# Kernel optimization log

Hardware: AMD Instinct MI355X
Metric: run time of the kernel (lower is better)

Reference implementation:

```python
import jax, jax.numpy as jnp
import numpy as np

D_MODEL = 1024
D_SAE = 16384
BATCH = 4096
EPS = 1e-8

def _layer_norm(v):
    # v: [B, D]; matches torch branch with keepdim=True
    mean = v.mean(axis=1, keepdims=True)
    var = ((v - mean) ** 2).mean(axis=1, keepdims=True)
    return (v - mean) / jnp.sqrt(var + EPS)

def setup_inputs() -> dict:
    key = jax.random.key(0)
    k1, k2 = jax.random.split(key)
    x = jax.random.normal(k1, (BATCH, 2 * D_MODEL), dtype=jnp.float32)
    # kaiming_uniform on [d_model, d_sae]: bound = sqrt(6 / fan_in), fan_in = d_sae (torch default mode='fan_in' on dim 1)
    bound = float(np.sqrt(6.0 / D_SAE))
    W_enc = jax.random.uniform(k2, (D_MODEL, D_SAE), dtype=jnp.float32, minval=-bound, maxval=bound)
    W_dec = W_enc.T  # init ties decoder to encoder transpose
    b_enc = jnp.zeros((D_SAE,), dtype=jnp.float32)
    b_dec = jnp.zeros((D_MODEL,), dtype=jnp.float32)
    return {"x": x, "W_enc": W_enc, "b_enc": b_enc, "W_dec": W_dec, "b_dec": b_dec, "k": 64}

def reference(x, W_enc, b_enc, W_dec, b_dec, k):
    B = x.shape[0]
    d_model = W_enc.shape[0]
    src = x[:, :d_model]
    tgt = x[:, d_model:]
    # standardize_method == 'layer_norm_and_diff_layer_norm'
    diff = _layer_norm(_layer_norm(tgt) - _layer_norm(src))  # [B, D]
    # encode
    acts = jax.nn.relu(diff @ W_enc + b_enc)  # [B, F]
    # batch top-k on decoder-norm-scaled scores
    dec_norms = jnp.linalg.norm(W_dec, axis=1)  # [F]
    flat_scores = (acts * dec_norms).reshape(-1)  # [B*F]
    _, topk_idx = jax.lax.top_k(flat_scores, k * B)
    mask = jnp.zeros_like(flat_scores).at[topk_idx].set(1.0).reshape(B, -1)
    sparse_acts = acts * mask  # [B, F]
    # decode
    recon = sparse_acts @ W_dec + b_dec  # [B, D]
    return recon
```

## Files before the change

### kernel.cpp

```cpp
#include <hip/hip_runtime.h>
#include <math.h>

#define D_MODEL 1024
#define D_SAE   16384
#define BATCH   4096
#define NTOT    (1ull * BATCH * D_SAE)
#define LN_EPS  1e-8
#define EPS_M   3e-4f
#define ROW_CAP 256
#define CAND_CAP  (4 * 1024 * 1024)
#define CAND2_CAP 65536

using bf16x8 = __attribute__((ext_vector_type(8))) short;
using f32x4  = __attribute__((ext_vector_type(4))) float;

__device__ inline unsigned short f2bf(float f) {
  unsigned u = __float_as_uint(f);
  return (unsigned short)((u + 0x7fffu + ((u >> 16) & 1u)) >> 16);
}
__device__ inline float bf2f(unsigned short h) {
  return __uint_as_float((unsigned)h << 16);
}

__device__ inline double blockReduceSum256(double v, double* lds) {
#pragma unroll
  for (int off = 32; off > 0; off >>= 1) v += __shfl_down(v, off, 64);
  int lane = threadIdx.x & 63, wid = threadIdx.x >> 6;
  __syncthreads();
  if (lane == 0) lds[wid] = v;
  __syncthreads();
  return lds[0] + lds[1] + lds[2] + lds[3];
}
__device__ inline int blockReduceSumInt256(int v, int* lds) {
#pragma unroll
  for (int off = 32; off > 0; off >>= 1) v += __shfl_down(v, off, 64);
  int lane = threadIdx.x & 63, wid = threadIdx.x >> 6;
  __syncthreads();
  if (lane == 0) lds[wid] = v;
  __syncthreads();
  return lds[0] + lds[1] + lds[2] + lds[3];
}

__device__ inline int wave_append(bool pred, int* counter) {
  unsigned long long m = __ballot(pred);
  int lane = threadIdx.x & 63;
  int pos = -1;
  if (m) {
    int ldr = __ffsll((long long)m) - 1;
    int base = 0;
    if (lane == ldr) base = atomicAdd(counter, __popcll(m));
    base = __shfl(base, ldr, 64);
    if (pred) pos = base + __popcll(m & ((1ull << lane) - 1ull));
  }
  return pos;
}

__device__ inline void hist_scan_desc(const int* __restrict__ hist, int nbins, int need,
                                      int& bsel, int& cumsel) {
  int t = threadIdx.x;
  int chunk = nbins >> 6;
  int topbase = nbins - t * chunk;
  int psum = 0;
  for (int i = 1; i <= chunk; ++i) psum += hist[topbase - i];
  int incl = psum;
#pragma unroll
  for (int off = 1; off < 64; off <<= 1) {
    int v = __shfl_up(incl, off, 64);
    if (t >= off) incl += v;
  }
  int excl = incl - psum;
  bool hit = (excl < need) && (excl + psum >= need);
  unsigned long long m = __ballot(hit);
  int tb = m ? (__ffsll((long long)m) - 1) : 63;
  int exb = __shfl(excl, tb, 64);
  int res_b = 0, res_c = 0;
  if (t == tb) {
    int c = exb;
    int b = nbins - tb * chunk - 1;
    int bend = b - chunk;
    for (; b > 0 && b > bend; --b) {
      int cc = hist[b];
      if (c + cc >= need) break;
      c += cc;
    }
    res_b = b; res_c = c;
  }
  bsel = __shfl(res_b, tb, 64);
  cumsel = __shfl(res_c, tb, 64);
}

__device__ inline void ln_row_fp64(const float* __restrict__ row, double* lds, double d[4]) {
  int t = threadIdx.x;
  float4 s4 = *(const float4*)(row + t * 4);
  float4 t4 = *(const float4*)(row + D_MODEL + t * 4);
  double s[4] = {s4.x, s4.y, s4.z, s4.w};
  double tt[4] = {t4.x, t4.y, t4.z, t4.w};
  double ms = blockReduceSum256(s[0] + s[1] + s[2] + s[3], lds) / D_MODEL;
  double mt = blockReduceSum256(tt[0] + tt[1] + tt[2] + tt[3], lds) / D_MODEL;
  double vs = 0, vt = 0;
#pragma unroll
  for (int i = 0; i < 4; i++) { double a = s[i] - ms; vs += a * a; a = tt[i] - mt; vt += a * a; }
  vs = blockReduceSum256(vs, lds) / D_MODEL;
  vt = blockReduceSum256(vt, lds) / D_MODEL;
  double rs = sqrt(vs + LN_EPS), rt = sqrt(vt + LN_EPS);
  double u[4];
#pragma unroll
  for (int i = 0; i < 4; i++) u[i] = (tt[i] - mt) / rt - (s[i] - ms) / rs;
  double mu = blockReduceSum256(u[0] + u[1] + u[2] + u[3], lds) / D_MODEL;
  double vu = 0;
#pragma unroll
  for (int i = 0; i < 4; i++) { double a = u[i] - mu; vu += a * a; }
  vu = blockReduceSum256(vu, lds) / D_MODEL;
  double ru = sqrt(vu + LN_EPS);
#pragma unroll
  for (int i = 0; i < 4; i++) d[i] = (u[i] - mu) / ru;
}

__global__ __launch_bounds__(256) void ln_kernel(const float* __restrict__ x,
                                                 short* __restrict__ Ahi, short* __restrict__ Alo) {
  __shared__ double lds[4];
  int b = blockIdx.x, t = threadIdx.x;
  double d[4];
  ln_row_fp64(x + (size_t)b * (2 * D_MODEL), lds, d);
  int mt = b >> 7, ml = b & 127;
  int ks = t >> 3, kc = (t >> 1) & 3, e0 = (t & 1) * 4;
  size_t base = ((((size_t)mt * 32 + ks) * 4 + kc) * 128 + ml) * 8 + e0;
  short h[4], l[4];
#pragma unroll
  for (int i = 0; i < 4; i++) {
    float f = (float)d[i];
    unsigned short hh = f2bf(f);
    h[i] = (short)hh;
    l[i] = (short)f2bf(f - bf2f(hh));
  }
  *(short4*)&Ahi[base] = make_short4(h[0], h[1], h[2], h[3]);
  *(short4*)&Alo[base] = make_short4(l[0], l[1], l[2], l[3]);
}

__global__ __launch_bounds__(256) void norm_kernel(const float* __restrict__ Wdec,
                                                   double* __restrict__ g64, float* __restrict__ g32) {
  int wv = threadIdx.x >> 6, lane = threadIdx.x & 63;
  int j = (blockIdx.x << 2) | wv;
  const float4* rowp = (const float4*)(Wdec + (size_t)j * D_MODEL);
  double a = 0;
#pragma unroll
  for (int q = 0; q < 4; ++q) {
    float4 w = rowp[lane + q * 64];
    a += (double)w.x * w.x + (double)w.y * w.y + (double)w.z * w.z + (double)w.w * w.w;
  }
#pragma unroll
  for (int off = 32; off > 0; off >>= 1) a += __shfl_down(a, off, 64);
  if (lane == 0) { double g = sqrt(a); g64[j] = g; g32[j] = (float)g; }
}

__global__ __launch_bounds__(256) void wsplit_kernel(const float* __restrict__ Wenc,
                                                     short* __restrict__ Whi, short* __restrict__ Wlo) {
  __shared__ short sh[4096];
  __shared__ short sl[4096];
  int blk = blockIdx.x;
  int nt = blk >> 5, ks = blk & 31;
  int t = threadIdx.x;
  int r = t >> 3;
  int cg = t & 7;
  int kc = r >> 3, e = r & 7;
  const float* src = Wenc + (size_t)(ks * 32 + r) * D_SAE + nt * 128 + cg;
#pragma unroll
  for (int j = 0; j < 16; ++j) {
    float f = src[j * 8];
    unsigned short hh = f2bf(f);
    short ll = (short)f2bf(f - bf2f(hh));
    int c = j * 8 + cg;
    sh[kc * 1024 + c * 8 + e] = (short)hh;
    sl[kc * 1024 + c * 8 + e] = ll;
  }
  __syncthreads();
  size_t obase = ((size_t)nt * 32 + ks) * 4096;
  *(float4*)&Whi[obase + t * 16]     = *(const float4*)&sh[t * 16];
  *(float4*)&Whi[obase + t * 16 + 8] = *(const float4*)&sh[t * 16 + 8];
  *(float4*)&Wlo[obase + t * 16]     = *(const float4*)&sl[t * 16];
  *(float4*)&Wlo[obase + t * 16 + 8] = *(const float4*)&sl[t * 16 + 8];
}

__global__ __launch_bounds__(256) void hist_gemm(
    const short* __restrict__ Whi, const short* __restrict__ Ahi,
    const float* __restrict__ benc, const float* __restrict__ g32,
    int* __restrict__ ghist) {
  __shared__ short sA[4096];
  __shared__ short sB[4096];
  __shared__ int h[4][2048];
  const int tid = threadIdx.x;
  const int lane = tid & 63;
  const int w = tid >> 6;
  const int wm = (w >> 1) * 64, wn = (w & 1) * 64;
  int lin = blockIdx.x;
  int mt = lin >> 7, nt = lin & 127;
  const int col0 = nt * 128;
  for (int i = tid; i < 8192; i += 256) ((int*)h)[i] = 0;
  const size_t atile = (size_t)mt * 131072;
  const size_t btile = (size_t)nt * 131072;
  f32x4 acc[4][4] = {};
  const int kcl = lane >> 4, l15 = lane & 15;

  float4 a0, a1, b0, b1;
  {
    const float4* ah4 = (const float4*)(Ahi + atile);
    const float4* bh4 = (const float4*)(Whi + btile);
    a0 = ah4[tid]; a1 = ah4[tid + 256];
    b0 = bh4[tid]; b1 = bh4[tid + 256];
  }
  for (int ks = 0; ks < 32; ++ks) {
    __syncthreads();
    *(float4*)&sA[(size_t)tid * 8] = a0;
    *(float4*)&sA[(size_t)(tid + 256) * 8] = a1;
    *(float4*)&sB[(size_t)tid * 8] = b0;
    *(float4*)&sB[(size_t)(tid + 256) * 8] = b1;
    __syncthreads();
    if (ks < 31) {
      const float4* ah4 = (const float4*)(Ahi + atile + (ks + 1) * 4096);
      const float4* bh4 = (const float4*)(Whi + btile + (ks + 1) * 4096);
      a0 = ah4[tid]; a1 = ah4[tid + 256];
      b0 = bh4[tid]; b1 = bh4[tid + 256];
    }
    bf16x8 ahf[4];
#pragma unroll
    for (int fm = 0; fm < 4; ++fm)
      ahf[fm] = *(const bf16x8*)&sA[(kcl * 128 + wm + fm * 16 + l15) * 8];
#pragma unroll
    for (int fn = 0; fn < 4; ++fn) {
      bf16x8 bh = *(const bf16x8*)&sB[(kcl * 128 + wn + fn * 16 + l15) * 8];
#pragma unroll
      for (int fm = 0; fm < 4; ++fm)
        acc[fm][fn] = __builtin_amdgcn_mfma_f32_16x16x32_bf16(ahf[fm], bh, acc[fm][fn], 0, 0, 0);
    }
  }
#pragma unroll
  for (int fn = 0; fn < 4; ++fn) {
    int col = col0 + wn + fn * 16 + l15;
    float g = g32[col], be = benc[col];
#pragma unroll
    for (int fm = 0; fm < 4; ++fm) {
#pragma unroll
      for (int r = 0; r < 4; ++r) {
        float z = acc[fm][fn][r] + be;
        float s = z > 0.f ? z * g : 0.f;
        unsigned bits = __float_as_uint(s);
        if (bits) atomicAdd(&h[w][bits >> 21], 1);
      }
    }
  }
  __syncthreads();
  for (int i = tid; i < 2048; i += 256) {
    int v = h[0][i] + h[1][i] + h[2][i] + h[3][i];
    if (v) atomicAdd(&ghist[i], v);
  }
}

__global__ __launch_bounds__(256, 3) void extract_gemm128(
    const short* __restrict__ Whi, const short* __restrict__ Wlo,
    const short* __restrict__ Ahi, const short* __restrict__ Alo,
    const float* __restrict__ benc, const float* __restrict__ g32,
    int* __restrict__ ctrl, int* __restrict__ cand_idx, float* __restrict__ cand_sc,
    int* __restrict__ ghist) {
  __shared__ short sA[8192];
  __shared__ short sB[8192];

  const int tid = threadIdx.x;
  const int lane = tid & 63;
  const int w = tid >> 6;
  const int wm = (w >> 1) * 64, wn = (w & 1) * 64;

  int lin = blockIdx.x;
  int xcd = lin & 7, j = lin >> 3;
  int mt = j & 31;
  int nt = (xcd << 4) | (j >> 5);
  const int row0 = mt * 128, col0 = nt * 128;

  const size_t atile = (size_t)mt * 131072;
  const size_t btile = (size_t)nt * 131072;

  f32x4 acc[4][4] = {};
  const int kcl = lane >> 4, l15 = lane & 15;

  float4 a0, a1, a2, a3, b0, b1, b2, b3;
  {
    const float4* ah4 = (const float4*)(Ahi + atile);
    const float4* al4 = (const float4*)(Alo + atile);
    const float4* bh4 = (const float4*)(Whi + btile);
    const float4* bl4 = (const float4*)(Wlo + btile);
    a0 = ah4[tid]; a1 = ah4[tid + 256];
    a2 = al4[tid]; a3 = al4[tid + 256];
    b0 = bh4[tid]; b1 = bh4[tid + 256];
    b2 = bl4[tid]; b3 = bl4[tid + 256];
  }

  for (int ks = 0; ks < 32; ++ks) {
    __syncthreads();
    *(float4*)&sA[(size_t)tid * 8] = a0;
    *(float4*)&sA[(size_t)(tid + 256) * 8] = a1;
    *(float4*)&sA[(size_t)(512 + tid) * 8] = a2;
    *(float4*)&sA[(size_t)(512 + tid + 256) * 8] = a3;
    *(float4*)&sB[(size_t)tid * 8] = b0;
    *(float4*)&sB[(size_t)(tid + 256) * 8] = b1;
    *(float4*)&sB[(size_t)(512 + tid) * 8] = b2;
    *(float4*)&sB[(size_t)(512 + tid + 256) * 8] = b3;
    __syncthreads();
    if (ks < 31) {
      const int o = (ks + 1) * 4096;
      const float4* ah4 = (const float4*)(Ahi + atile + o);
      const float4* al4 = (const float4*)(Alo + atile + o);
      const float4* bh4 = (const float4*)(Whi + btile + o);
      const float4* bl4 = (const float4*)(Wlo + btile + o);
      a0 = ah4[tid]; a1 = ah4[tid + 256];
      a2 = al4[tid]; a3 = al4[tid + 256];
      b0 = bh4[tid]; b1 = bh4[tid + 256];
      b2 = bl4[tid]; b3 = bl4[tid + 256];
    }
    bf16x8 ahf[4], alf[4];
#pragma unroll
    for (int fm = 0; fm < 4; ++fm) {
      int off = (kcl * 128 + wm + fm * 16 + l15) * 8;
      ahf[fm] = *(const bf16x8*)&sA[off];
      alf[fm] = *(const bf16x8*)&sA[4096 + off];
    }
#pragma unroll
    for (int fn = 0; fn < 4; ++fn) {
      int boff = (kcl * 128 + wn + fn * 16 + l15) * 8;
      bf16x8 bh = *(const bf16x8*)&sB[boff];
      bf16x8 bl = *(const bf16x8*)&sB[4096 + boff];
#pragma unroll
      for (int fm = 0; fm < 4; ++fm) {
        acc[fm][fn] = __builtin_amdgcn_mfma_f32_16x16x32_bf16(ahf[fm], bh, acc[fm][fn], 0, 0, 0);
        acc[fm][fn] = __builtin_amdgcn_mfma_f32_16x16x32_bf16(alf[fm], bh, acc[fm][fn], 0, 0, 0);
        acc[fm][fn] = __builtin_amdgcn_mfma_f32_16x16x32_bf16(ahf[fm], bl, acc[fm][fn], 0, 0, 0);
      }
    }
  }

  int* hh = (int*)sA;
  const int l4r = lane >> 4;
  unsigned thrBits = (unsigned)ctrl[1];
  __syncthreads();
  for (int i = tid; i < 2050; i += 256) hh[i] = 0;
  __syncthreads();
  int cnt = 0;
#pragma unroll
  for (int fn = 0; fn < 4; ++fn) {
    int col = col0 + wn + fn * 16 + l15;
    float g = g32[col], be = benc[col];
#pragma unroll
    for (int fm = 0; fm < 4; ++fm) {
#pragma unroll
      for (int r = 0; r < 4; ++r) {
        float z = acc[fm][fn][r] + be;
        float s = z > 0.f ? z * g : 0.f;
        unsigned bits = __float_as_uint(s);
        if (bits >= thrBits) { cnt++; atomicAdd(&hh[bits >> 21], 1); }
      }
    }
  }
  int my = 0;
  if (cnt) my = atomicAdd(&hh[2048], cnt);
  __syncthreads();
  if (tid == 0) hh[2049] = atomicAdd(&ctrl[2], hh[2048]);
  for (int i = tid; i < 2048; i += 256)
    if (hh[i]) atomicAdd(&ghist[i], hh[i]);
  __syncthreads();
  int pos = hh[2049] + my;
#pragma unroll
  for (int fn = 0; fn < 4; ++fn) {
    int col = col0 + wn + fn * 16 + l15;
    float g = g32[col], be = benc[col];
#pragma unroll
    for (int fm = 0; fm < 4; ++fm) {
      int rowb = row0 + wm + fm * 16 + l4r * 4;
#pragma unroll
      for (int r = 0; r < 4; ++r) {
        float z = acc[fm][fn][r] + be;
        float s = z > 0.f ? z * g : 0.f;
        if (__float_as_uint(s) >= thrBits) {
          if (pos < CAND_CAP) { cand_idx[pos] = (rowb + r) * D_SAE + col; cand_sc[pos] = s; }
          pos++;
        }
      }
    }
  }
}

template <int MODE>
__global__ __launch_bounds__(256) void mfma_gemm(
    const float* __restrict__ Wenc,
    const short* __restrict__ Ahi, const short* __restrict__ Alo,
    const float* __restrict__ benc, const float* __restrict__ g32,
    int* __restrict__ ghist, int* __restrict__ ctrl,
    int* __restrict__ cand_idx, float* __restrict__ cand_sc) {
  __shared__ short sA[8192];
  __shared__ short sB[8192];
  __shared__ int h[(MODE == 0) ? 2048 : 2];
  const int tid = threadIdx.x;
  const int lane = tid & 63;
  const int w = tid >> 6;
  const int wm = (w >> 1) * 64, wn = (w & 1) * 64;
  int lin = blockIdx.x;
  int mt, nt;
  if (MODE == 0) { mt = lin >> 7; nt = lin & 127; }
  else { int xcd = lin & 7, j = lin >> 3; mt = j & 31; nt = (xcd << 4) | (j >> 5); }
  const int row0 = mt * 128, col0 = nt * 128;
  if (MODE == 0) { for (int i = tid; i < 2048; i += 256) h[i] = 0; }
  else if (tid == 0) h[0] = 0;
  const int nl = tid & 127;
  const int half = tid >> 7;
  const float* wbase = Wenc + (size_t)col0 + nl;
  const size_t atile = (size_t)mt * 131072;
  f32x4 acc[4][4] = {};
  const int kcl = lane >> 4, l15 = lane & 15;
  float4 a0, a1, a2, a3;
  float bfv[16];
  {
    const float4* ah4 = (const float4*)(Ahi + atile);
    const float4* al4 = (const float4*)(Alo + atile);
    a0 = ah4[tid]; a1 = ah4[tid + 256];
    a2 = al4[tid]; a3 = al4[tid + 256];
#pragma unroll
    for (int p = 0; p < 4; ++p)
#pragma unroll
      for (int i = 0; i < 4; ++i)
        bfv[p * 4 + i] = wbase[(size_t)(p * 8 + half * 4 + i) * D_SAE];
  }
  for (int ks = 0; ks < 32; ++ks) {
    short hb[16], lb[16];
#pragma unroll
    for (int q = 0; q < 16; ++q) {
      unsigned short hh = f2bf(bfv[q]);
      hb[q] = (short)hh;
      lb[q] = (short)f2bf(bfv[q] - bf2f(hh));
    }
    __syncthreads();
    *(float4*)&sA[(size_t)tid * 8] = a0;
    *(float4*)&sA[(size_t)(tid + 256) * 8] = a1;
    *(float4*)&sA[(size_t)(512 + tid) * 8] = a2;
    *(float4*)&sA[(size_t)(512 + tid + 256) * 8] = a3;
#pragma unroll
    for (int p = 0; p < 4; ++p) {
      int boff = p * 1024 + nl * 8 + half * 4;
      *(short4*)&sB[boff] = make_short4(hb[p * 4], hb[p * 4 + 1], hb[p * 4 + 2], hb[p * 4 + 3]);
      *(short4*)&sB[4096 + boff] = make_short4(lb[p * 4], lb[p * 4 + 1], lb[p * 4 + 2], lb[p * 4 + 3]);
    }
    __syncthreads();
    if (ks < 31) {
      const float4* ah4 = (const float4*)(Ahi + atile + (ks + 1) * 4096);
      const float4* al4 = (const float4*)(Alo + atile + (ks + 1) * 4096);
      a0 = ah4[tid]; a1 = ah4[tid + 256];
      a2 = al4[tid]; a3 = al4[tid + 256];
      const int k0n = (ks + 1) * 32;
#pragma unroll
      for (int p = 0; p < 4; ++p)
#pragma unroll
        for (int i = 0; i < 4; ++i)
          bfv[p * 4 + i] = wbase[(size_t)(k0n + p * 8 + half * 4 + i) * D_SAE];
    }
    bf16x8 ahf[4], alf[4];
#pragma unroll
    for (int fm = 0; fm < 4; ++fm) {
      int off = (kcl * 128 + wm + fm * 16 + l15) * 8;
      ahf[fm] = *(const bf16x8*)&sA[off];
      alf[fm] = *(const bf16x8*)&sA[4096 + off];
    }
#pragma unroll
    for (int fn = 0; fn < 4; ++fn) {
      int boff = (kcl * 128 + wn + fn * 16 + l15) * 8;
      bf16x8 bh = *(const bf16x8*)&sB[boff];
      bf16x8 bl = *(const bf16x8*)&sB[4096 + boff];
#pragma unroll
      for (int fm = 0; fm < 4; ++fm) {
        acc[fm][fn] = __builtin_amdgcn_mfma_f32_16x16x32_bf16(ahf[fm], bh, acc[fm][fn], 0, 0, 0);
        acc[fm][fn] = __builtin_amdgcn_mfma_f32_16x16x32_bf16(alf[fm], bh, acc[fm][fn], 0, 0, 0);
        acc[fm][fn] = __builtin_amdgcn_mfma_f32_16x16x32_bf16(ahf[fm], bl, acc[fm][fn], 0, 0, 0);
      }
    }
  }
  const int l4r = lane >> 4;
  if (MODE == 0) {
#pragma unroll
    for (int fn = 0; fn < 4; ++fn) {
      int col = col0 + wn + fn * 16 + l15;
      float g = g32[col], be = benc[col];
#pragma unroll
      for (int fm = 0; fm < 4; ++fm) {
#pragma unroll
        for (int r = 0; r < 4; ++r) {
          float z = acc[fm][fn][r] + be;
          float s = z > 0.f ? z * g : 0.f;
          unsigned bits = __float_as_uint(s);
          if (bits) atomicAdd(&h[bits >> 21], 1);
        }
      }
    }
    __syncthreads();
    for (int i = tid; i < 2048; i += 256)
      if (h[i]) atomicAdd(&ghist[i], h[i]);
  } else {
    unsigned thrBits = (unsigned)ctrl[1];
    int cnt = 0;
#pragma unroll
    for (int fn = 0; fn < 4; ++fn) {
      int col = col0 + wn + fn * 16 + l15;
      float g = g32[col], be = benc[col];
#pragma unroll
      for (int fm = 0; fm < 4; ++fm) {
#pragma unroll
        for (int r = 0; r < 4; ++r) {
          float z = acc[fm][fn][r] + be;
          float s = z > 0.f ? z * g : 0.f;
          cnt += (__float_as_uint(s) >= thrBits) ? 1 : 0;
        }
      }
    }
    int my = 0;
    if (cnt) my = atomicAdd(&h[0], cnt);
    __syncthreads();
    if (tid == 0) h[1] = atomicAdd(&ctrl[2], h[0]);
    __syncthreads();
    int pos = h[1] + my;
#pragma unroll
    for (int fn = 0; fn < 4; ++fn) {
      int col = col0 + wn + fn * 16 + l15;
      float g = g32[col], be = benc[col];
#pragma unroll
      for (int fm = 0; fm < 4; ++fm) {
        int rowb = row0 + wm + fm * 16 + l4r * 4;
#pragma unroll
        for (int r = 0; r < 4; ++r) {
          float z = acc[fm][fn][r] + be;
          float s = z > 0.f ? z * g : 0.f;
          if (__float_as_uint(s) >= thrBits) {
            if (pos < CAND_CAP) { cand_idx[pos] = (rowb + r) * D_SAE + col; cand_sc[pos] = s; }
            pos++;
          }
        }
      }
    }
  }
}

__global__ void find_coarse_kernel(const int* __restrict__ gh, int* ctrl,
                                   const int* __restrict__ kptr, int sub) {
  long long kB = (long long)kptr[0] * BATCH;
  long long needl = (kB + 500000 + sub - 1) / sub;
  long long fl = 720000 / sub;
  if (needl < fl) needl = fl;
  int b, cum;
  hist_scan_desc(gh, 2048, (int)needl, b, cum);
  if (threadIdx.x == 0) {
    long long est_incl = (long long)sub * (cum + gh[b]);
    if (est_incl > 3500000LL && (long long)sub * cum >= kB + 120000LL) b = b + 1;
    ctrl[1] = (int)(((unsigned)b) << 21);
  }
}

__global__ __launch_bounds__(256) void chist_kernel(const float* __restrict__ cand_sc,
                                                    const int* __restrict__ ctrl,
                                                    int* __restrict__ ghist, int pass) {
  __shared__ int h[2048];
  int nb = (pass == 2) ? 1024 : 2048;
  for (int i = threadIdx.x; i < nb; i += 256) h[i] = 0;
  __syncthreads();
  int n = ctrl[2]; if (n > CAND_CAP) n = CAND_CAP;
  unsigned sel1 = 0, sel22 = 0;
  if (pass == 1) sel1 = (unsigned)ctrl[3];
  if (pass == 2) sel22 = ((unsigned)ctrl[3] << 11) | (unsigned)ctrl[5];
  for (int i = blockIdx.x * 256 + threadIdx.x; i < n; i += gridDim.x * 256) {
    unsigned bits = __float_as_uint(cand_sc[i]);
    if (pass == 0) atomicAdd(&h[bits >> 21], 1);
    else if (pass == 1) { if ((bits >> 21) == sel1) atomicAdd(&h[(bits >> 10) & 0x7FFu], 1); }
    else { if ((bits >> 10) == sel22) atomicAdd(&h[bits & 0x3FFu], 1); }
  }
  __syncthreads();
  for (int i = threadIdx.x; i < nb; i += 256)
    if (h[i]) atomicAdd(&ghist[i], h[i]);
}

__global__ void cfind_kernel(const int* __restrict__ hist, int* ctrl,
                             const int* __restrict__ kptr, int pass) {
  int kB = kptr[0] * BATCH;
  int need, nbins;
  if (pass == 0)      { need = kB;                       nbins = 2048; }
  else if (pass == 1) { need = kB - ctrl[4];             nbins = 2048; }
  else                { need = kB - ctrl[4] - ctrl[6];   nbins = 1024; }
  int b, cum;
  hist_scan_desc(hist, nbins, need, b, cum);
  if (threadIdx.x == 0) {
    if (pass == 0)      { ctrl[3] = b; ctrl[4] = cum; }
    else if (pass == 1) { ctrl[5] = b; ctrl[6] = cum; }
    else {
      unsigned vbits = ((unsigned)ctrl[3] << 21) | ((unsigned)ctrl[5] << 10) | (unsigned)b;
      float V = __uint_as_float(vbits);
      float* cf = (float*)ctrl;
      cf[8] = V; cf[9] = V + EPS_M; cf[10] = V - EPS_M;
    }
  }
}

__global__ __launch_bounds__(256) void band_kernel(const int* __restrict__ cand_idx,
    const float* __restrict__ cand_sc, const float* __restrict__ g32,
    int* ctrl, int* row_cnt, int* row_feat, float* row_act, int* cand2_idx) {
  const float* cf = (const float*)ctrl;
  float hi = cf[9], lo = cf[10];
  int n = ctrl[2]; if (n > CAND_CAP) n = CAND_CAP;
  int lane = threadIdx.x & 63;
  int defc = 0;
  for (int i = blockIdx.x * 256 + threadIdx.x; i < n; i += gridDim.x * 256) {
    float s = cand_sc[i];
    int flat = cand_idx[i];
    if (s > hi) {
      int b = flat >> 14, j = flat & (D_SAE - 1);
      int p = atomicAdd(&row_cnt[b], 1);
      if (p < ROW_CAP) { row_feat[b * ROW_CAP + p] = j; row_act[b * ROW_CAP + p] = s / g32[j]; }
      defc++;
    }
    bool isc = (s <= hi) && (s >= lo);
    int pos = wave_append(isc, &ctrl[12]);
    if (isc && pos >= 0 && pos < CAND2_CAP) cand2_idx[pos] = flat;
  }
#pragma unroll
  for (int off = 32; off > 0; off >>= 1) defc += __shfl_down(defc, off, 64);
  if (lane == 0 && defc) atomicAdd(&ctrl[11], defc);
}

__global__ __launch_bounds__(256) void cand2_score_kernel(const int* __restrict__ ctrl,
    const int* __restrict__ cand2_idx, const float* __restrict__ x,
    const float* __restrict__ Wdec, const float* __restrict__ benc,
    const double* __restrict__ g64, double* __restrict__ cand2_sc) {
  __shared__ double lds[4];
  int n2 = ctrl[12]; if (n2 > CAND2_CAP) n2 = CAND2_CAP;
  int t = threadIdx.x;
  for (int c = blockIdx.x; c < n2; c += gridDim.x) {
    int flat = cand2_idx[c];
    int b = flat >> 14, j = flat & (D_SAE - 1);
    double d[4];
    ln_row_fp64(x + (size_t)b * (2 * D_MODEL), lds, d);
    float4 w4 = *(const float4*)(Wdec + (size_t)j * D_MODEL + t * 4);
    double a = d[0] * (double)w4.x + d[1] * (double)w4.y + d[2] * (double)w4.z + d[3] * (double)w4.w;
    double z = blockReduceSum256(a, lds) + (double)benc[j];
    double sc = z > 0 ? z * g64[j] : 0.0;
    if (t == 0) cand2_sc[c] = sc;
  }
}

__global__ __launch_bounds__(256) void cand2_rank_kernel(const int* __restrict__ ctrl,
    const int* __restrict__ cand2_idx, const double* __restrict__ cand2_sc,
    const double* __restrict__ g64, const int* __restrict__ kptr,
    int* row_cnt, int* row_feat, float* row_act) {
  __shared__ int lds[4];
  int n2 = ctrl[12]; if (n2 > CAND2_CAP) n2 = CAND2_CAP;
  int kB = kptr[0] * BATCH;
  int fill = kB - ctrl[11];
  int t = threadIdx.x;
  for (int c = blockIdx.x; c < n2; c += gridDim.x) {
    double sc = cand2_sc[c];
    int fc = cand2_idx[c];
    int cnt = 0;
    for (int y = t; y < n2; y += 256) {
      double sy = cand2_sc[y];
      if (sy > sc || (sy == sc && cand2_idx[y] < fc)) cnt++;
    }
    cnt = blockReduceSumInt256(cnt, lds);
    if (t == 0 && cnt < fill) {
      int b = fc >> 14, j = fc & (D_SAE - 1);
      int p = atomicAdd(&row_cnt[b], 1);
      if (p < ROW_CAP) { row_feat[b * ROW_CAP + p] = j; row_act[b * ROW_CAP + p] = (float)(sc / g64[j]); }
    }
  }
}

__global__ __launch_bounds__(256) void recon_kernel(const int* __restrict__ row_cnt,
    const int* __restrict__ row_feat, const float* __restrict__ row_act,
    const float* __restrict__ Wdec, const float* __restrict__ bdec, float* __restrict__ out) {
  int b = blockIdx.x, t = threadIdx.x;
  float4 acc0 = *(const float4*)&bdec[t * 4];
  float4 acc1 = make_float4(0.f, 0.f, 0.f, 0.f);
  int n = row_cnt[b]; if (n > ROW_CAP) n = ROW_CAP;
  const int* rf = row_feat + (size_t)b * ROW_CAP;
  const float* ra = row_act + (size_t)b * ROW_CAP;
  int p = 0;
  for (; p + 2 <= n; p += 2) {
    int j0 = rf[p], j1 = rf[p + 1];
    float v0 = ra[p], v1 = ra[p + 1];
    float4 w0 = *(const float4*)(Wdec + (size_t)j0 * D_MODEL + t * 4);
    float4 w1 = *(const float4*)(Wdec + (size_t)j1 * D_MODEL + t * 4);
    acc0.x += v0 * w0.x; acc0.y += v0 * w0.y; acc0.z += v0 * w0.z; acc0.w += v0 * w0.w;
    acc1.x += v1 * w1.x; acc1.y += v1 * w1.y; acc1.z += v1 * w1.z; acc1.w += v1 * w1.w;
  }
  if (p < n) {
    int j0 = rf[p]; float v0 = ra[p];
    float4 w0 = *(const float4*)(Wdec + (size_t)j0 * D_MODEL + t * 4);
    acc0.x += v0 * w0.x; acc0.y += v0 * w0.y; acc0.z += v0 * w0.z; acc0.w += v0 * w0.w;
  }
  acc0.x += acc1.x; acc0.y += acc1.y; acc0.z += acc1.z; acc0.w += acc1.w;
  *(float4*)(out + (size_t)b * D_MODEL + t * 4) = acc0;
}

extern "C" void kernel_launch(void* const* d_in, const int* in_sizes, int n_in,
                              void* d_out, int out_size, void* d_ws, size_t ws_size,
                              hipStream_t stream) {
  const float* x    = (const float*)d_in[0];
  const float* Wenc = (const float*)d_in[1];
  const float* benc = (const float*)d_in[2];
  const float* Wdec = (const float*)d_in[3];
  const float* bdec = (const float*)d_in[4];
  const int*   kptr = (const int*)d_in[5];
  float* out = (float*)d_out;

  char* ws = (char*)d_ws;
  size_t off = 0;
  short*  Ahi       = (short*)(ws + off);  off += (size_t)BATCH * D_MODEL * 2;
  short*  Alo       = (short*)(ws + off);  off += (size_t)BATCH * D_MODEL * 2;
  int*    cand_idx  = (int*)(ws + off);    off += (size_t)CAND_CAP * 4;
  float*  cand_sc   = (float*)(ws + off);  off += (size_t)CAND_CAP * 4;
  int*    row_feat  = (int*)(ws + off);    off += (size_t)BATCH * ROW_CAP * 4;
  float*  row_act   = (float*)(ws + off);  off += (size_t)BATCH * ROW_CAP * 4;
  int*    cand2_idx = (int*)(ws + off);    off += (size_t)CAND2_CAP * 4;
  double* cand2_sc  = (double*)(ws + off); off += (size_t)CAND2_CAP * 8;
  double* g64       = (double*)(ws + off); off += (size_t)D_SAE * 8;
  float*  g32       = (float*)(ws + off);  off += (size_t)D_SAE * 4;
  char*   zbase     = ws + off;
  int* ghist   = (int*)(zbase);
  int* h1      = (int*)(zbase + 8192);
  int* h2      = (int*)(zbase + 16384);
  int* h3      = (int*)(zbase + 24576);
  int* ctrl    = (int*)(zbase + 28672);
  int* row_cnt = (int*)(zbase + 28928);
  size_t zbytes = 28928 + (size_t)BATCH * 4;
  size_t small_need = off + zbytes;
  if (small_need > ws_size) return;

  size_t big_off = (small_need + 255) & ~(size_t)255;
  short* Whi = (short*)(ws + big_off);
  short* Wlo = Whi + (size_t)D_MODEL * D_SAE;
  size_t big_need = big_off + (size_t)D_MODEL * D_SAE * 4;
  const bool big = (big_need <= ws_size);

  hipMemsetAsync(zbase, 0, zbytes, stream);

  ln_kernel<<<BATCH, 256, 0, stream>>>(x, Ahi, Alo);
  norm_kernel<<<D_SAE / 4, 256, 0, stream>>>(Wdec, g64, g32);
  if (big) {
    wsplit_kernel<<<4096, 256, 0, stream>>>(Wenc, Whi, Wlo);
    hist_gemm<<<512, 256, 0, stream>>>(Whi, Ahi, benc, g32, ghist);
    find_coarse_kernel<<<1, 64, 0, stream>>>(ghist, ctrl, kptr, 8);
    extract_gemm128<<<4096, 256, 0, stream>>>(Whi, Wlo, Ahi, Alo, benc, g32, ctrl, cand_idx, cand_sc, h1);
  } else {
    mfma_gemm<0><<<256, 256, 0, stream>>>(Wenc, Ahi, Alo, benc, g32, ghist, ctrl, nullptr, nullptr);
    find_coarse_kernel<<<1, 64, 0, stream>>>(ghist, ctrl, kptr, 16);
    mfma_gemm<1><<<4096, 256, 0, stream>>>(Wenc, Ahi, Alo, benc, g32, nullptr, ctrl, cand_idx, cand_sc);
    chist_kernel<<<1024, 256, 0, stream>>>(cand_sc, ctrl, h1, 0);
  }
  cfind_kernel<<<1, 64, 0, stream>>>(h1, ctrl, kptr, 0);
  chist_kernel<<<1024, 256, 0, stream>>>(cand_sc, ctrl, h2, 1);
  cfind_kernel<<<1, 64, 0, stream>>>(h2, ctrl, kptr, 1);
  chist_kernel<<<1024, 256, 0, stream>>>(cand_sc, ctrl, h3, 2);
  cfind_kernel<<<1, 64, 0, stream>>>(h3, ctrl, kptr, 2);
  band_kernel<<<1024, 256, 0, stream>>>(cand_idx, cand_sc, g32, ctrl, row_cnt, row_feat, row_act, cand2_idx);
  cand2_score_kernel<<<4096, 256, 0, stream>>>(ctrl, cand2_idx, x, Wdec, benc, g64, cand2_sc);
  cand2_rank_kernel<<<2048, 256, 0, stream>>>(ctrl, cand2_idx, cand2_sc, g64, kptr, row_cnt, row_feat, row_act);
  recon_kernel<<<BATCH, 256, 0, stream>>>(row_cnt, row_feat, row_act, Wdec, bdec, out);
}
```

Before: 762.7 us.

## Use wave-per-row layer norm, remap GEMM tile order, halve histogram sampling

The layer-norm kernel now handles one row per wavefront (four rows per block) using shuffle-xor reductions instead of block-level LDS reductions, and writes 16-byte vectorized bf16 hi/lo stores. The extract GEMM block-to-tile mapping is changed so each XCD gets a contiguous group of M tiles instead of N tiles, which changes how A and W tiles are shared in each XCD's L2. The histogram GEMM launches half as many blocks, with the coarse-threshold scale factor doubled to match. This sampling change trades estimate accuracy for less work and could grow the candidate set if the threshold becomes looser.

```diff
diff --git a/kernel.cpp b/kernel.cpp
--- a/kernel.cpp
+++ b/kernel.cpp
@@ -118,23 +118,69 @@
 
 __global__ __launch_bounds__(256) void ln_kernel(const float* __restrict__ x,
                                                  short* __restrict__ Ahi, short* __restrict__ Alo) {
-  __shared__ double lds[4];
-  int b = blockIdx.x, t = threadIdx.x;
-  double d[4];
-  ln_row_fp64(x + (size_t)b * (2 * D_MODEL), lds, d);
-  int mt = b >> 7, ml = b & 127;
-  int ks = t >> 3, kc = (t >> 1) & 3, e0 = (t & 1) * 4;
-  size_t base = ((((size_t)mt * 32 + ks) * 4 + kc) * 128 + ml) * 8 + e0;
-  short h[4], l[4];
-#pragma unroll
-  for (int i = 0; i < 4; i++) {
-    float f = (float)d[i];
-    unsigned short hh = f2bf(f);
-    h[i] = (short)hh;
-    l[i] = (short)f2bf(f - bf2f(hh));
-  }
-  *(short4*)&Ahi[base] = make_short4(h[0], h[1], h[2], h[3]);
-  *(short4*)&Alo[base] = make_short4(l[0], l[1], l[2], l[3]);
+  int wv = threadIdx.x >> 6, lane = threadIdx.x & 63;
+  int b = (blockIdx.x << 2) | wv;
+  const float* row = x + (size_t)b * (2 * D_MODEL);
+  float s[16], t[16];
+  const float4* s4p = (const float4*)(row + lane * 16);
+  const float4* t4p = (const float4*)(row + D_MODEL + lane * 16);
+  double sum_s = 0, sum_t = 0;
+#pragma unroll
+  for (int q = 0; q < 4; ++q) {
+    float4 a = s4p[q], c = t4p[q];
+    s[q * 4 + 0] = a.x; s[q * 4 + 1] = a.y; s[q * 4 + 2] = a.z; s[q * 4 + 3] = a.w;
+    t[q * 4 + 0] = c.x; t[q * 4 + 1] = c.y; t[q * 4 + 2] = c.z; t[q * 4 + 3] = c.w;
+  }
+#pragma unroll
+  for (int i = 0; i < 16; ++i) { sum_s += s[i]; sum_t += t[i]; }
+#pragma unroll
+  for (int off = 1; off < 64; off <<= 1) {
+    sum_s += __shfl_xor(sum_s, off, 64);
+    sum_t += __shfl_xor(sum_t, off, 64);
+  }
+  double ms = sum_s / D_MODEL, mt_ = sum_t / D_MODEL;
+  double vs = 0, vt = 0;
+#pragma unroll
+  for (int i = 0; i < 16; ++i) {
+    double a = s[i] - ms; vs += a * a;
+    double c = t[i] - mt_; vt += c * c;
+  }
+#pragma unroll
+  for (int off = 1; off < 64; off <<= 1) {
+    vs += __shfl_xor(vs, off, 64);
+    vt += __shfl_xor(vt, off, 64);
+  }
+  double rs = sqrt(vs / D_MODEL + LN_EPS), rt = sqrt(vt / D_MODEL + LN_EPS);
+  double u[16], su = 0;
+#pragma unroll
+  for (int i = 0; i < 16; ++i) { u[i] = (t[i] - mt_) / rt - (s[i] - ms) / rs; su += u[i]; }
+#pragma unroll
+  for (int off = 1; off < 64; off <<= 1) su += __shfl_xor(su, off, 64);
+  double mu = su / D_MODEL, vu = 0;
+#pragma unroll
+  for (int i = 0; i < 16; ++i) { double a = u[i] - mu; vu += a * a; }
+#pragma unroll
+  for (int off = 1; off < 64; off <<= 1) vu += __shfl_xor(vu, off, 64);
+  double ru = sqrt(vu / D_MODEL + LN_EPS);
+  int mtb = b >> 7, ml = b & 127;
+#pragma unroll
+  for (int blk8 = 0; blk8 < 2; ++blk8) {
+    short h8[8], l8[8];
+#pragma unroll
+    for (int e = 0; e < 8; ++e) {
+      int i = blk8 * 8 + e;
+      double dd = (u[i] - mu) / ru;
+      float f = (float)dd;
+      unsigned short hh = f2bf(f);
+      h8[e] = (short)hh;
+      l8[e] = (short)f2bf(f - bf2f(hh));
+    }
+    int gi = lane * 16 + blk8 * 8;
+    int ks = gi >> 5, kc = (gi >> 3) & 3;
+    size_t base = ((((size_t)mtb * 32 + ks) * 4 + kc) * 128 + ml) * 8;
+    *(float4*)&Ahi[base] = *(float4*)h8;
+    *(float4*)&Alo[base] = *(float4*)l8;
+  }
 }
 
 __global__ __launch_bounds__(256) void norm_kernel(const float* __restrict__ Wdec,
@@ -271,8 +317,8 @@
 
   int lin = blockIdx.x;
   int xcd = lin & 7, j = lin >> 3;
-  int mt = j & 31;
-  int nt = (xcd << 4) | (j >> 5);
+  int mt = (xcd << 2) | (j & 3);
+  int nt = j >> 2;
   const int row0 = mt * 128, col0 = nt * 128;
 
   const size_t atile = (size_t)mt * 131072;
@@ -741,12 +787,12 @@
 
   hipMemsetAsync(zbase, 0, zbytes, stream);
 
-  ln_kernel<<<BATCH, 256, 0, stream>>>(x, Ahi, Alo);
+  ln_kernel<<<BATCH / 4, 256, 0, stream>>>(x, Ahi, Alo);
   norm_kernel<<<D_SAE / 4, 256, 0, stream>>>(Wdec, g64, g32);
   if (big) {
     wsplit_kernel<<<4096, 256, 0, stream>>>(Wenc, Whi, Wlo);
-    hist_gemm<<<512, 256, 0, stream>>>(Whi, Ahi, benc, g32, ghist);
-    find_coarse_kernel<<<1, 64, 0, stream>>>(ghist, ctrl, kptr, 8);
+    hist_gemm<<<256, 256, 0, stream>>>(Whi, Ahi, benc, g32, ghist);
+    find_coarse_kernel<<<1, 64, 0, stream>>>(ghist, ctrl, kptr, 16);
     extract_gemm128<<<4096, 256, 0, stream>>>(Whi, Wlo, Ahi, Alo, benc, g32, ctrl, cand_idx, cand_sc, h1);
   } else {
     mfma_gemm<0><<<256, 256, 0, stream>>>(Wenc, Ahi, Alo, benc, g32, ghist, ctrl, nullptr, nullptr);
```

Result: faster. 733.7 us (-3.8%).
